# Optimization experiments

Measured on AMD Instinct MI355X. Metric: run time of the kernel, lower is better.

## Reference

```python
import jax, jax.numpy as jnp
import numpy as np

N, C, T, V = 128, 256, 48, 25
CR = C // 16
SEG = 3
BN_EPS = 1e-5


def setup_inputs() -> dict:
    key = jax.random.key(0)
    ks = jax.random.split(key, 8)
    s = lambda k, shape: jax.random.normal(k, shape, dtype=jnp.float32) * 0.05
    return {
        "x": jax.random.normal(ks[0], (N, C, T, V), dtype=jnp.float32),
        "w_sq": s(ks[1], (CR, C)),   # me_squeeze 1x1 conv weight [out,in]
        "b_sq": s(ks[2], (CR,)),
        "gamma": jnp.ones((CR,), jnp.float32),   # BN weight
        "beta": jnp.zeros((CR,), jnp.float32),   # BN bias
        "rmean": jnp.zeros((CR,), jnp.float32),  # BN running mean
        "rvar": jnp.ones((CR,), jnp.float32),    # BN running var
        "w_c1": s(ks[3], (CR, CR)),  # me_conv1 1x1 conv weight
        "b_c1": s(ks[4], (CR,)),
        "w_ex": s(ks[5], (C, CR)),   # me_expand 1x1 conv weight
        "b_ex": s(ks[6], (C,)),
    }


def reference(x, w_sq, b_sq, gamma, beta, rmean, rvar, w_c1, b_c1, w_ex, b_ex):
    n, c, t, v = x.shape
    nb = (n * t) // SEG
    cr = w_sq.shape[0]
    # 1x1 squeeze conv + BatchNorm (eval mode, running stats) -> [n, cr, t, v]
    y = jnp.einsum('nctv,rc->nrtv', x, w_sq) + b_sq[None, :, None, None]
    scale = gamma / jnp.sqrt(rvar + BN_EPS)
    y = y * scale[None, :, None, None] + (beta - rmean * scale)[None, :, None, None]
    # 1x1 conv on squeezed features (shifted branch)
    y1 = jnp.einsum('nrtv,sr->nstv', y, w_c1) + b_c1[None, :, None, None]
    # regroup consecutive frames into segments of SEG along time: (n*t) -> (nb, SEG)
    yseg = y.transpose(0, 2, 1, 3).reshape(nb, SEG, cr, v)
    y1seg = y1.transpose(0, 2, 1, 3).reshape(nb, SEG, cr, v)
    # temporal difference: conv(frame k+1) - frame k, zero-pad last frame of each segment
    diff = y1seg[:, 1:] - yseg[:, :SEG - 1]                    # [nb, SEG-1, cr, v]
    diff = jnp.pad(diff, ((0, 0), (0, 1), (0, 0), (0, 0)))     # [nb, SEG, cr, v]
    x_me = diff.reshape(n, t, cr, v).transpose(0, 2, 1, 3)     # [n, cr, t, v]
    # adaptive avg pool over joints (v -> 1), expand conv, sigmoid gate
    m = jnp.mean(x_me, axis=-1, keepdims=True)                 # [n, cr, t, 1]
    gate = jax.nn.sigmoid(jnp.einsum('nrtu,cr->nctu', m, w_ex) + b_ex[None, :, None, None])
    return x * gate
```

## Files before the change

kernel.cpp:

```cpp
#include <hip/hip_runtime.h>

#define N_  128
#define C_  256
#define T_  48
#define V_  25

typedef float v4f __attribute__((ext_vector_type(4)));

__global__ __launch_bounds__(512, 4) void k_fused7(
    const float* __restrict__ x,
    const float* __restrict__ wsq, const float* __restrict__ bsq,
    const float* __restrict__ gamma, const float* __restrict__ beta,
    const float* __restrict__ rmean, const float* __restrict__ rvar,
    const float* __restrict__ wc1, const float* __restrict__ bc1,
    const float* __restrict__ wex, const float* __restrict__ bex,
    float* __restrict__ out)
{
    __shared__ v4f   buf[2][1280];
    __shared__ float xb[3072];
    __shared__ float gs[3072];
    __shared__ float ybn[192], y1[192], mv[192];

    const int tid = threadIdx.x;
    const int wv  = tid >> 6;
    const int ln  = tid & 63;

    const unsigned bid = blockIdx.x;
    const unsigned o   = (bid & 7u) * 64u + (bid >> 3);
    const unsigned n   = o >> 2;
    const unsigned qd  = o & 3u;

    const v4f* x4 = (const v4f*)x + (size_t)n * 76800u + qd * 75u;
    v4f*       o4 = (v4f*)out     + (size_t)n * 76800u + qd * 75u;

    auto stage = [&](int cg, v4f* dst) {
        const v4f* xq = x4 + cg * 4800;
        v4f tmp[10];
        #pragma unroll
        for (int i = 0; i < 10; ++i) {
            int s  = i * 128 + (wv - 6) * 64 + ln;
            int sc = (s < 1200) ? s : 1199;
            int c  = sc / 75, k = sc - c * 75;
            tmp[i] = xq[c * 300 + k];
        }
        #pragma unroll
        for (int i = 0; i < 10; ++i)
            dst[i * 128 + (wv - 6) * 64 + ln] = tmp[i];
    };

    if (wv >= 6) stage(0, buf[0]);
    __syncthreads();
    for (int cg = 0; cg < 16; ++cg) {
        if (wv >= 6 && cg < 15) stage(cg + 1, buf[(cg + 1) & 1]);
        if (tid < 192) {
            int cl = tid / 12, t = tid - cl * 12;
            const float* bp = (const float*)&buf[cg & 1][cl * 75] + t * 25;
            float s = 0.f;
            #pragma unroll
            for (int v = 0; v < 25; ++v) s += bp[v];
            xb[(cg * 16 + cl) * 12 + t] = s;
        }
        __syncthreads();
    }

    for (int e = tid; e < 1536; e += 512) {
        int g = e & 7, q = e >> 3, t = q >> 4, r = q & 15;
        const float* wrow = wsq + r * 256 + g * 32;
        float acc = 0.f;
        #pragma unroll 8
        for (int i = 0; i < 32; ++i) acc += xb[(g * 32 + i) * 12 + t] * wrow[i];
        gs[e] = acc;
    }
    __syncthreads();

    if (wv == 0) {
        #pragma unroll
        for (int j = 0; j < 3; ++j) {
            int q = ln + j * 64, r = q & 15;
            float acc = 0.f;
            #pragma unroll
            for (int g = 0; g < 8; ++g) acc += gs[q * 8 + g];
            float sc = gamma[r] * rsqrtf(rvar[r] + 1e-5f);
            ybn[q] = acc * (0.04f * sc) + (bsq[r] * sc + beta[r] - rmean[r] * sc);
        }
        #pragma unroll
        for (int j = 0; j < 3; ++j) {
            int q = ln + j * 64, t = q >> 4, s = q & 15;
            float acc = bc1[s];
            #pragma unroll
            for (int r = 0; r < 16; ++r) acc += ybn[t * 16 + r] * wc1[s * 16 + r];
            y1[q] = acc;
        }
        #pragma unroll
        for (int j = 0; j < 3; ++j) {
            int q = ln + j * 64, t = q >> 4;
            mv[q] = ((t % 3) < 2) ? (y1[q + 16] - ybn[q]) : 0.f;
        }
    }
    __syncthreads();

    {
        int c = tid & 255, half = tid >> 8;
        float wexr[16];
        #pragma unroll
        for (int r = 0; r < 16; ++r) wexr[r] = wex[c * 16 + r];
        float be = bex[c];
        #pragma unroll
        for (int t = half * 6; t < half * 6 + 6; ++t) {
            float a = be;
            #pragma unroll
            for (int r = 0; r < 16; ++r) a += mv[t * 16 + r] * wexr[r];
            gs[c * 12 + t] = 1.f / (1.f + expf(-a));
        }
    }
    __syncthreads();

    #pragma unroll 4
    for (int it = 0; it < 38; ++it) {
        int j = it * 512 + tid;
        if (j < 19200) {
            unsigned c = ((unsigned)j * 55926u) >> 22;
            int k = j - (int)c * 75;
            v4f v = x4[c * 300 + k];
            int m0  = k * 4;
            int t0  = (m0 * 41) >> 10;
            int t3  = ((m0 + 3) * 41) >> 10;
            int rem = m0 - t0 * 25;
            float g0 = gs[c * 12 + t0];
            float g3 = gs[c * 12 + t3];
            v4f ov;
            ov.x = v.x * g0;
            ov.y = v.y * ((rem + 1 < 25) ? g0 : g3);
            ov.z = v.z * ((rem + 2 < 25) ? g0 : g3);
            ov.w = v.w * ((rem + 3 < 25) ? g0 : g3);
            __builtin_nontemporal_store(ov, &o4[c * 300 + k]);
        }
    }
}

extern "C" void kernel_launch(void* const* d_in, const int* in_sizes, int n_in,
                              void* d_out, int out_size, void* d_ws, size_t ws_size,
                              hipStream_t stream) {
    const float* x     = (const float*)d_in[0];
    const float* wsq   = (const float*)d_in[1];
    const float* bsq   = (const float*)d_in[2];
    const float* gamma = (const float*)d_in[3];
    const float* beta  = (const float*)d_in[4];
    const float* rmean = (const float*)d_in[5];
    const float* rvar  = (const float*)d_in[6];
    const float* wc1   = (const float*)d_in[7];
    const float* bc1   = (const float*)d_in[8];
    const float* wex   = (const float*)d_in[9];
    const float* bex   = (const float*)d_in[10];

    k_fused7<<<512, 512, 0, stream>>>(x, wsq, bsq, gamma, beta,
                                      rmean, rvar, wc1, bc1, wex, bex,
                                      (float*)d_out);
}
```

Before: 85.59 us.

## Overlap squeeze-conv accumulation with staged channel reduction and pad LDS rows

The squeeze 1x1 conv accumulation moves into the staged channel loop. A third thread group (192-383) accumulates the previous channel group's contributions while loader warps fetch the next group and reducer threads sum joints. The squeeze weights are transposed into padded LDS, and staging rows are padded to 77 to reduce bank conflicts. The separate xb-times-wsq pass and its partial-sum reduction go away, and the gate buffer reuses the staging buffer, so LDS use does not grow much. The intent is to hide the squeeze GEMV behind memory loads, but the kernel is mostly bandwidth-bound, so the gain may be small.

```diff
diff --git a/kernel.cpp b/kernel.cpp
--- a/kernel.cpp
+++ b/kernel.cpp
@@ -1,13 +1,8 @@
 #include <hip/hip_runtime.h>
-
-#define N_  128
-#define C_  256
-#define T_  48
-#define V_  25
 
 typedef float v4f __attribute__((ext_vector_type(4)));
 
-__global__ __launch_bounds__(512, 4) void k_fused7(
+__global__ __launch_bounds__(512, 4) void k_fused8(
     const float* __restrict__ x,
     const float* __restrict__ wsq, const float* __restrict__ bsq,
     const float* __restrict__ gamma, const float* __restrict__ beta,
@@ -16,89 +11,94 @@
     const float* __restrict__ wex, const float* __restrict__ bex,
     float* __restrict__ out)
 {
-    __shared__ v4f   buf[2][1280];
-    __shared__ float xb[3072];
-    __shared__ float gs[3072];
+    __shared__ v4f   buf[2][16 * 77];
+    __shared__ float xb[12 * 256];
+    __shared__ float wsqL[256 * 17];
     __shared__ float ybn[192], y1[192], mv[192];
 
     const int tid = threadIdx.x;
-    const int wv  = tid >> 6;
-    const int ln  = tid & 63;
+    const unsigned bid = blockIdx.x;
+    const unsigned o = (bid & 7u) * 64u + (bid >> 3);
+    const unsigned n = o >> 2;
+    const unsigned q = o & 3u;
 
-    const unsigned bid = blockIdx.x;
-    const unsigned o   = (bid & 7u) * 64u + (bid >> 3);
-    const unsigned n   = o >> 2;
-    const unsigned qd  = o & 3u;
+    const v4f* x4 = (const v4f*)x + (size_t)n * 76800u + q * 75u;
+    v4f*       o4 = (v4f*)out     + (size_t)n * 76800u + q * 75u;
 
-    const v4f* x4 = (const v4f*)x + (size_t)n * 76800u + qd * 75u;
-    v4f*       o4 = (v4f*)out     + (size_t)n * 76800u + qd * 75u;
+    float* gsb = (float*)buf;
+
+    float acc = 0.f;
 
     auto stage = [&](int cg, v4f* dst) {
-        const v4f* xq = x4 + cg * 4800;
+        const int pt = tid - 384;
         v4f tmp[10];
         #pragma unroll
         for (int i = 0; i < 10; ++i) {
-            int s  = i * 128 + (wv - 6) * 64 + ln;
+            int s = i * 128 + pt;
             int sc = (s < 1200) ? s : 1199;
-            int c  = sc / 75, k = sc - c * 75;
-            tmp[i] = xq[c * 300 + k];
+            int c = sc / 75, k = sc - c * 75;
+            tmp[i] = x4[(cg * 16 + c) * 300 + k];
         }
         #pragma unroll
-        for (int i = 0; i < 10; ++i)
-            dst[i * 128 + (wv - 6) * 64 + ln] = tmp[i];
+        for (int i = 0; i < 10; ++i) {
+            int s = i * 128 + pt;
+            int sc = (s < 1200) ? s : 1199;
+            int c = sc / 75, k = sc - c * 75;
+            dst[c * 77 + k] = tmp[i];
+        }
+    };
+    auto reduceC = [&](int cg) {
+        int t = tid >> 4, cl = tid & 15;
+        const float* bp = (const float*)&buf[cg & 1][cl * 77] + t * 25;
+        float s = 0.f;
+        #pragma unroll
+        for (int v = 0; v < 25; ++v) s += bp[v];
+        xb[t * 256 + cg * 16 + cl] = s;
+    };
+    auto accumB1 = [&](int cg) {
+        int u = tid - 192, t = u >> 4, r = u & 15;
+        #pragma unroll
+        for (int i = 0; i < 16; ++i) {
+            int c = cg * 16 + i;
+            acc += xb[t * 256 + c] * wsqL[c * 17 + r];
+        }
     };
 
-    if (wv >= 6) stage(0, buf[0]);
+    #pragma unroll
+    for (int it = 0; it < 8; ++it) {
+        int j = it * 512 + tid;
+        wsqL[(j & 255) * 17 + (j >> 8)] = wsq[j];
+    }
+    if (tid >= 384) stage(0, buf[0]);
     __syncthreads();
-    for (int cg = 0; cg < 16; ++cg) {
-        if (wv >= 6 && cg < 15) stage(cg + 1, buf[(cg + 1) & 1]);
-        if (tid < 192) {
-            int cl = tid / 12, t = tid - cl * 12;
-            const float* bp = (const float*)&buf[cg & 1][cl * 75] + t * 25;
-            float s = 0.f;
-            #pragma unroll
-            for (int v = 0; v < 25; ++v) s += bp[v];
-            xb[(cg * 16 + cl) * 12 + t] = s;
-        }
+
+    for (int i = 0; i < 16; ++i) {
+        if (tid >= 384) { if (i < 15) stage(i + 1, buf[(i + 1) & 1]); }
+        else if (tid < 192) reduceC(i);
+        else if (i > 0) accumB1(i - 1);
         __syncthreads();
     }
 
-    for (int e = tid; e < 1536; e += 512) {
-        int g = e & 7, q = e >> 3, t = q >> 4, r = q & 15;
-        const float* wrow = wsq + r * 256 + g * 32;
-        float acc = 0.f;
-        #pragma unroll 8
-        for (int i = 0; i < 32; ++i) acc += xb[(g * 32 + i) * 12 + t] * wrow[i];
-        gs[e] = acc;
+    if (tid >= 192 && tid < 384) {
+        accumB1(15);
+        int u = tid - 192, r = u & 15;
+        float sc = gamma[r] * rsqrtf(rvar[r] + 1e-5f);
+        ybn[u] = acc * (0.04f * sc) + (bsq[r] * sc + beta[r] - rmean[r] * sc);
     }
     __syncthreads();
-
-    if (wv == 0) {
+    if (tid < 192) {
+        int t = tid >> 4, s = tid & 15;
+        float a = bc1[s];
         #pragma unroll
-        for (int j = 0; j < 3; ++j) {
-            int q = ln + j * 64, r = q & 15;
-            float acc = 0.f;
-            #pragma unroll
-            for (int g = 0; g < 8; ++g) acc += gs[q * 8 + g];
-            float sc = gamma[r] * rsqrtf(rvar[r] + 1e-5f);
-            ybn[q] = acc * (0.04f * sc) + (bsq[r] * sc + beta[r] - rmean[r] * sc);
-        }
-        #pragma unroll
-        for (int j = 0; j < 3; ++j) {
-            int q = ln + j * 64, t = q >> 4, s = q & 15;
-            float acc = bc1[s];
-            #pragma unroll
-            for (int r = 0; r < 16; ++r) acc += ybn[t * 16 + r] * wc1[s * 16 + r];
-            y1[q] = acc;
-        }
-        #pragma unroll
-        for (int j = 0; j < 3; ++j) {
-            int q = ln + j * 64, t = q >> 4;
-            mv[q] = ((t % 3) < 2) ? (y1[q + 16] - ybn[q]) : 0.f;
-        }
+        for (int r = 0; r < 16; ++r) a += ybn[t * 16 + r] * wc1[s * 16 + r];
+        y1[tid] = a;
     }
     __syncthreads();
-
+    if (tid < 192) {
+        int t = tid >> 4;
+        mv[tid] = ((t % 3) < 2) ? (y1[tid + 16] - ybn[tid]) : 0.f;
+    }
+    __syncthreads();
     {
         int c = tid & 255, half = tid >> 8;
         float wexr[16];
@@ -110,7 +110,7 @@
             float a = be;
             #pragma unroll
             for (int r = 0; r < 16; ++r) a += mv[t * 16 + r] * wexr[r];
-            gs[c * 12 + t] = 1.f / (1.f + expf(-a));
+            gsb[c * 12 + t] = 1.f / (1.f + expf(-a));
         }
     }
     __syncthreads();
@@ -126,8 +126,8 @@
             int t0  = (m0 * 41) >> 10;
             int t3  = ((m0 + 3) * 41) >> 10;
             int rem = m0 - t0 * 25;
-            float g0 = gs[c * 12 + t0];
-            float g3 = gs[c * 12 + t3];
+            float g0 = gsb[c * 12 + t0];
+            float g3 = gsb[c * 12 + t3];
             v4f ov;
             ov.x = v.x * g0;
             ov.y = v.y * ((rem + 1 < 25) ? g0 : g3);
@@ -153,7 +153,7 @@
     const float* wex   = (const float*)d_in[9];
     const float* bex   = (const float*)d_in[10];
 
-    k_fused7<<<512, 512, 0, stream>>>(x, wsq, bsq, gamma, beta,
+    k_fused8<<<512, 512, 0, stream>>>(x, wsq, bsq, gamma, beta,
                                       rmean, rvar, wc1, bc1, wex, bex,
                                       (float*)d_out);
 }
```

New measurement: 77.02 us. -10.0%, faster.
